# Optimization experiments

Measured on AMD Instinct MI355X. Metric: run time of the kernel, lower is better.

Reference implementation:

```python
import jax, jax.numpy as jnp
import numpy as np

D_MODEL = 2048
NUM_Q_HEADS = 32
NUM_KV_HEADS = 8
HEAD_DIM = D_MODEL // NUM_Q_HEADS  # 64
NUM_GROUPS = NUM_Q_HEADS // NUM_KV_HEADS  # 4


def setup_inputs() -> dict:
    key = jax.random.key(0)
    ks = jax.random.split(key, 9)
    s = 1.0 / np.sqrt(D_MODEL)
    x = jax.random.normal(ks[0], (2, 2048, D_MODEL), dtype=jnp.float32)
    Wq = jax.random.uniform(ks[1], (D_MODEL, NUM_Q_HEADS * HEAD_DIM), jnp.float32, -s, s)
    bq = jax.random.uniform(ks[2], (NUM_Q_HEADS * HEAD_DIM,), jnp.float32, -s, s)
    Wk = jax.random.uniform(ks[3], (D_MODEL, NUM_KV_HEADS * HEAD_DIM), jnp.float32, -s, s)
    bk = jax.random.uniform(ks[4], (NUM_KV_HEADS * HEAD_DIM,), jnp.float32, -s, s)
    Wv = jax.random.uniform(ks[5], (D_MODEL, NUM_KV_HEADS * HEAD_DIM), jnp.float32, -s, s)
    bv = jax.random.uniform(ks[6], (NUM_KV_HEADS * HEAD_DIM,), jnp.float32, -s, s)
    Wo = jax.random.uniform(ks[7], (D_MODEL, D_MODEL), jnp.float32, -s, s)
    bo = jax.random.uniform(ks[8], (D_MODEL,), jnp.float32, -s, s)
    return {"x": x, "Wq": Wq, "bq": bq, "Wk": Wk, "bk": bk,
            "Wv": Wv, "bv": bv, "Wo": Wo, "bo": bo}


def reference(x, Wq, bq, Wk, bk, Wv, bv, Wo, bo):
    B, T, C = x.shape
    Hkv, G, Dh = NUM_KV_HEADS, NUM_GROUPS, HEAD_DIM
    # projections
    q = (x @ Wq + bq).reshape(B, T, Hkv, G, Dh)   # group G query heads per kv head
    k = (x @ Wk + bk).reshape(B, T, Hkv, Dh)
    v = (x @ Wv + bv).reshape(B, T, Hkv, Dh)
    scale = 1.0 / np.sqrt(Dh).astype(np.float32)
    # scores: [B, Hkv, G, T, T] (kv head broadcast over its G query heads)
    scores = jnp.einsum('btkgd,bskd->bkgts', q, k) * scale
    attn = jax.nn.softmax(scores, axis=-1)
    out = jnp.einsum('bkgts,bskd->btkgd', attn, v).reshape(B, T, C)
    return out @ Wo + bo
```

## Files before the change

kernel.cpp:

```cpp
#include <hip/hip_runtime.h>
#include <cstdint>
#include <cstddef>
#include <math.h>

typedef uint16_t bf16;
typedef __attribute__((ext_vector_type(8))) __bf16 bf16x8;
typedef __attribute__((ext_vector_type(2))) float f32x2;
typedef __attribute__((ext_vector_type(4))) float f32x4;
typedef __attribute__((ext_vector_type(16))) float f32x16;

#define MFMA16(a,b,c) __builtin_amdgcn_mfma_f32_16x16x32_bf16((a),(b),(c),0,0,0)
#define MFMA32(a,b,c) __builtin_amdgcn_mfma_f32_32x32x16_bf16((a),(b),(c),0,0,0)

__device__ __forceinline__ uint16_t f2bf(float f){
  uint32_t u = __float_as_uint(f);
  return (uint16_t)((u + 0x7fffu + ((u >> 16) & 1u)) >> 16);
}
__device__ __forceinline__ uint32_t pk2(float lo, float hi){
  return (uint32_t)f2bf(lo) | ((uint32_t)f2bf(hi) << 16);
}

__device__ __forceinline__ void gload_lds16(const void* g, void* l){
  __builtin_amdgcn_global_load_lds((const __attribute__((address_space(1))) void*)g,
                                   (__attribute__((address_space(3))) void*)l, 16, 0, 0);
}

__global__ void k_convert(const float* __restrict__ in, bf16* __restrict__ out, int n){
  int i = (blockIdx.x * 256 + threadIdx.x) * 4;
  if (i >= n) return;
  float4 v = *reinterpret_cast<const float4*>(in + i);
  uint32_t lo = pk2(v.x, v.y);
  uint32_t hi = pk2(v.z, v.w);
  uint2 pkv = make_uint2(lo, hi);
  *reinterpret_cast<uint2*>(out + i) = pkv;
}

__global__ void k_transposeW(const float* __restrict__ in, bf16* __restrict__ out, int R, int C){
  __shared__ float tile[64][65];
  int c0 = blockIdx.x * 64, r0 = blockIdx.y * 64;
  int t = threadIdx.x;
  int fx = t & 15, fy = t >> 4;
  #pragma unroll
  for (int i = 0; i < 4; i++){
    int r = fy + i*16;
    float4 v = *reinterpret_cast<const float4*>(in + (size_t)(r0 + r)*C + c0 + fx*4);
    tile[r][fx*4+0] = v.x; tile[r][fx*4+1] = v.y;
    tile[r][fx*4+2] = v.z; tile[r][fx*4+3] = v.w;
  }
  __syncthreads();
  int gx = t & 7, gy = t >> 3;
  #pragma unroll
  for (int i = 0; i < 2; i++){
    int c = gy + i*32;
    int rr = gx*8;
    union { bf16 h[8]; uint4 u; } pk_;
    #pragma unroll
    for (int j = 0; j < 8; j++) pk_.h[j] = f2bf(tile[rr+j][c]);
    *reinterpret_cast<uint4*>(out + (size_t)(c0 + c)*R + r0 + rr) = pk_.u;
  }
}

__device__ __forceinline__ void gemm128_core(
    const bf16* __restrict__ Abase, const bf16* __restrict__ Btbase,
    int lda, int ldb, int K, bf16* As, bf16* Bs, f32x4 acc[4][4])
{
  const int tid = threadIdx.x;
  const int wid = tid >> 6, lane = tid & 63;
  const int wr = wid >> 1, wc = wid & 1;
  const int lr = lane & 15, lg = lane >> 4;
  const f32x4 vzero = {0.f, 0.f, 0.f, 0.f};

  #pragma unroll
  for (int m = 0; m < 4; m++)
    #pragma unroll
    for (int n = 0; n < 4; n++)
      acc[m][n] = vzero;

  int srcA[4], srcB[4], dOff[4];
  #pragma unroll
  for (int i = 0; i < 4; i++){
    int d = i*4096 + wid*1024 + lane*16;
    int row = d >> 7, sp = (d >> 4) & 7;
    int sl = sp ^ (row & 7);
    srcA[i] = row * lda + sl * 8;
    srcB[i] = row * ldb + sl * 8;
    dOff[i] = i*4096 + wid*1024;
  }

  for (int k0 = 0; k0 < K; k0 += 64){
    #pragma unroll
    for (int i = 0; i < 4; i++)
      gload_lds16(Abase + k0 + srcA[i], (char*)As + dOff[i]);
    #pragma unroll
    for (int i = 0; i < 4; i++)
      gload_lds16(Btbase + k0 + srcB[i], (char*)Bs + dOff[i]);
    __syncthreads();
    #pragma unroll
    for (int ks = 0; ks < 2; ks++){
      bf16x8 af[4], bfr[4];
      #pragma unroll
      for (int m = 0; m < 4; m++){
        int row = wr*64 + m*16 + lr;
        int sp = (ks*4 + lg) ^ (row & 7);
        af[m] = *reinterpret_cast<const bf16x8*>(As + row*64 + sp*8);
      }
      #pragma unroll
      for (int n = 0; n < 4; n++){
        int row = wc*64 + n*16 + lr;
        int sp = (ks*4 + lg) ^ (row & 7);
        bfr[n] = *reinterpret_cast<const bf16x8*>(Bs + row*64 + sp*8);
      }
      #pragma unroll
      for (int m = 0; m < 4; m++)
        #pragma unroll
        for (int n = 0; n < 4; n++)
          acc[m][n] = MFMA16(af[m], bfr[n], acc[m][n]);
    }
    __syncthreads();
  }
}

__global__ __launch_bounds__(256, 2) void k_qkv(
    const bf16* __restrict__ xb,
    const bf16* __restrict__ WqT, const bf16* __restrict__ WkT, const bf16* __restrict__ WvT,
    const float* __restrict__ bq, const float* __restrict__ bk, const float* __restrict__ bv,
    bf16* __restrict__ qo, bf16* __restrict__ ko, bf16* __restrict__ vtp)
{
  __shared__ __align__(16) bf16 As[128*64];
  __shared__ __align__(16) bf16 Bs[128*64];
  int by = blockIdx.y;
  const bf16* Bt; const float* bias; int mode; int y = 0; float scale = 1.f;
  if (by < 16){      Bt = WqT + (size_t)by*128*2048;      bias = bq + by*128; mode = 0; y = by;   scale = 0.18033688011112042f; }
  else if (by < 20){ y = by-16; Bt = WkT + (size_t)y*128*2048; bias = bk + y*128; mode = 1; }
  else {             y = by-20; Bt = WvT + (size_t)y*128*2048; bias = bv + y*128; mode = 2; }
  int m0 = blockIdx.x * 128;
  f32x4 acc[4][4];
  gemm128_core(xb + (size_t)m0*2048, Bt, 2048, 2048, 2048, As, Bs, acc);
  const int tid = threadIdx.x, wid = tid >> 6, lane = tid & 63;
  const int wr = wid >> 1, wc = wid & 1, lr = lane & 15, lg = lane >> 4;
  if (mode == 2){
    #pragma unroll
    for (int n = 0; n < 4; n++){
      int cl = wc*64 + n*16 + lr;
      float bb = bias[cl];
      #pragma unroll
      for (int m = 0; m < 4; m++){
        int row0 = m0 + wr*64 + m*16 + lg*4;
        int bi = row0 >> 11, tl = row0 & 2047;
        union { bf16 h[4]; uint2 u; } pk_;
        #pragma unroll
        for (int r = 0; r < 4; r++) pk_.h[r] = f2bf(acc[m][n][r] + bb);
        *reinterpret_cast<uint2*>(vtp + ((size_t)bi*512 + y*128 + cl)*2048 + tl) = pk_.u;
      }
    }
  } else {
    bf16* outp = (mode == 0) ? (qo + y*128) : (ko + y*128);
    int ldc = (mode == 0) ? 2048 : 512;
    #pragma unroll
    for (int n = 0; n < 4; n++){
      int col = wc*64 + n*16 + lr;
      float bb = bias[col];
      #pragma unroll
      for (int m = 0; m < 4; m++)
        #pragma unroll
        for (int r = 0; r < 4; r++){
          int row = m0 + wr*64 + m*16 + lg*4 + r;
          outp[(size_t)row*ldc + col] = f2bf((acc[m][n][r] + bb) * scale);
        }
    }
  }
}

__global__ __launch_bounds__(256, 2) void k_oproj(
    const bf16* __restrict__ ab, const bf16* __restrict__ WoT,
    const float* __restrict__ bo, float* __restrict__ outp)
{
  __shared__ __align__(16) bf16 As[128*64];
  __shared__ __align__(16) bf16 Bs[128*64];
  int m0 = blockIdx.x * 128, n0 = blockIdx.y * 128;
  f32x4 acc[4][4];
  gemm128_core(ab + (size_t)m0*2048, WoT + (size_t)n0*2048, 2048, 2048, 2048, As, Bs, acc);
  const int tid = threadIdx.x, wid = tid >> 6, lane = tid & 63;
  const int wr = wid >> 1, wc = wid & 1, lr = lane & 15, lg = lane >> 4;
  #pragma unroll
  for (int n = 0; n < 4; n++){
    int col = n0 + wc*64 + n*16 + lr;
    float bb = bo[col];
    #pragma unroll
    for (int m = 0; m < 4; m++)
      #pragma unroll
      for (int r = 0; r < 4; r++){
        int row = m0 + wr*64 + m*16 + lg*4 + r;
        outp[(size_t)row*2048 + col] = acc[m][n][r] + bb;
      }
  }
}

__global__ __launch_bounds__(512, 2) void k_flash(
    const bf16* __restrict__ q, const bf16* __restrict__ kmat,
    const bf16* __restrict__ vt, bf16* __restrict__ ao)
{
  __shared__ __align__(16) char lds[98304];
  const int tid = threadIdx.x;
  const int wid = tid >> 6, lane = tid & 63;
  const int l31 = lane & 31, hi = lane >> 5;
  const int bh = blockIdx.y;
  const int b = bh >> 5, hq = bh & 31, kvh = hq >> 2;
  const int qt = blockIdx.x;
  const int qrow0 = b*2048 + qt*512 + wid*64;

  bf16x8 qf[2][4];
  #pragma unroll
  for (int g = 0; g < 2; g++){
    const bf16* qrow = q + (size_t)(qrow0 + g*32 + l31)*2048 + hq*64 + hi*8;
    #pragma unroll
    for (int t = 0; t < 4; t++)
      qf[g][t] = *reinterpret_cast<const bf16x8*>(qrow + t*16);
  }

  f32x16 oacc[2][2];
  #pragma unroll
  for (int g = 0; g < 2; g++)
    #pragma unroll
    for (int n = 0; n < 2; n++)
      #pragma unroll
      for (int r = 0; r < 16; r++) oacc[g][n][r] = 0.f;
  float rsg[2][2];
  rsg[0][0]=0.f; rsg[0][1]=0.f; rsg[1][0]=0.f; rsg[1][1]=0.f;
  const f32x16 zv = {0.f,0.f,0.f,0.f,0.f,0.f,0.f,0.f,0.f,0.f,0.f,0.f,0.f,0.f,0.f,0.f};

  const int r7 = l31 & 7;
  int A[4];
  #pragma unroll
  for (int j = 0; j < 4; j++)
    A[j] = l31*128 + (((2*j + hi) ^ r7) << 4);

  const bf16* kbase = kmat + (size_t)b*2048*512 + kvh*64;
  const bf16* vbase = vt + ((size_t)b*512 + kvh*64)*2048;

  int kSrc[2], vSrc[2];
  const int dOf = wid*1024;
  #pragma unroll
  for (int i = 0; i < 2; i++){
    int kdb = i*8192 + tid*16;
    int krow = kdb >> 7, ksp = (kdb >> 4) & 7, ksl = ksp ^ (krow & 7);
    kSrc[i] = krow*512 + ksl*8;
    int o = tid*16;
    int vrow = o >> 7, vsp = (o >> 4) & 7, vsl = vsp ^ (vrow & 7);
    vSrc[i] = vrow*2048 + i*64 + vsl*8;
  }

  #define STAGE(bo, st_) do { \
    const bf16* kb_ = kbase + (size_t)(st_)*128*512; \
    const bf16* vb_ = vbase + (st_)*128; \
    gload_lds16(kb_ + kSrc[0], lds + (bo) + dOf); \
    gload_lds16(kb_ + kSrc[1], lds + (bo) + 8192 + dOf); \
    gload_lds16(vb_ + vSrc[0], lds + 49152 + (bo) + dOf); \
    gload_lds16(vb_ + vSrc[1], lds + 49152 + (bo) + 8192 + dOf); \
  } while(0)

  #define LDK(j, imm) (*reinterpret_cast<const bf16x8*>(lds + kOff + A[j] + (imm)))
  #define LDV(j, imm) (*reinterpret_cast<const bf16x8*>(lds + 49152 + kOff + A[j] + (imm)))

  STAGE(0, 0);
  STAGE(16384, 1);

  int kOff = 0;
  int sOff = 32768;
  for (int st = 0; st < 16; st++){
    if (st == 15) asm volatile("s_waitcnt vmcnt(0)" ::: "memory");
    else          asm volatile("s_waitcnt vmcnt(4)" ::: "memory");
    __builtin_amdgcn_sched_barrier(0);
    __builtin_amdgcn_s_barrier();
    __builtin_amdgcn_sched_barrier(0);
    if (st < 14){
      STAGE(sOff, st+2);
      sOff = (sOff == 32768) ? 0 : sOff + 16384;
    }

    #pragma unroll
    for (int c = 0; c < 2; c++){
      f32x16 sc[2][2];
      __builtin_amdgcn_s_setprio(1);
      #pragma unroll
      for (int t = 0; t < 4; t++){
        bf16x8 af0 = LDK(t, c*8192);
        bf16x8 af1 = LDK(t, c*8192 + 4096);
        if (t == 0){
          sc[0][0] = MFMA32(af0, qf[0][0], zv);
          sc[1][0] = MFMA32(af0, qf[1][0], zv);
          sc[0][1] = MFMA32(af1, qf[0][0], zv);
          sc[1][1] = MFMA32(af1, qf[1][0], zv);
        } else {
          sc[0][0] = MFMA32(af0, qf[0][t], sc[0][0]);
          sc[1][0] = MFMA32(af0, qf[1][t], sc[1][0]);
          sc[0][1] = MFMA32(af1, qf[0][t], sc[0][1]);
          sc[1][1] = MFMA32(af1, qf[1][t], sc[1][1]);
        }
      }
      __builtin_amdgcn_s_setprio(0);

      uint32_t pw[2][2][8];
      #pragma unroll
      for (int g = 0; g < 2; g++){
        #pragma unroll
        for (int n = 0; n < 2; n++)
          #pragma unroll
          for (int j = 0; j < 8; j++){
            float plo = __builtin_amdgcn_exp2f(sc[g][n][2*j]);
            float phi = __builtin_amdgcn_exp2f(sc[g][n][2*j+1]);
            rsg[g][j & 1] += plo + phi;
            asm("v_cvt_pk_bf16_f32 %0, %1, %2" : "=v"(pw[g][n][j]) : "v"(plo), "v"(phi));
          }
        #pragma unroll
        for (int n = 0; n < 2; n++)
          #pragma unroll
          for (int h = 0; h < 2; h++){
            asm volatile("v_permlane32_swap_b32 %0, %1" : "+v"(pw[g][n][h*4+0]), "+v"(pw[g][n][h*4+2]));
            asm volatile("v_permlane32_swap_b32 %0, %1" : "+v"(pw[g][n][h*4+1]), "+v"(pw[g][n][h*4+3]));
          }
      }

      __builtin_amdgcn_s_setprio(1);
      #pragma unroll
      for (int kk = 0; kk < 4; kk++){
        int n = kk >> 1, h = kk & 1;
        union { uint32_t w[4]; bf16x8 v; } pa0, pa1;
        #pragma unroll
        for (int w_ = 0; w_ < 4; w_++){ pa0.w[w_] = pw[0][n][h*4+w_]; pa1.w[w_] = pw[1][n][h*4+w_]; }
        #pragma unroll
        for (int nd = 0; nd < 2; nd++){
          bf16x8 vf = LDV(kk, c*8192 + nd*4096);
          oacc[0][nd] = MFMA32(pa0.v, vf, oacc[0][nd]);
          oacc[1][nd] = MFMA32(pa1.v, vf, oacc[1][nd]);
        }
      }
      __builtin_amdgcn_s_setprio(0);
    }
    kOff = (kOff == 32768) ? 0 : kOff + 16384;
  }
  #undef STAGE
  #undef LDK
  #undef LDV

  #pragma unroll
  for (int g = 0; g < 2; g++){
    float rs = rsg[g][0] + rsg[g][1];
    float l = rs + __shfl_xor(rs, 32);
    float linv = 1.f / l;
    float lv[16];
    #pragma unroll
    for (int r = 0; r < 16; r++){
      int qi = (r & 3) + 8*(r >> 2) + 4*hi;
      lv[r] = __shfl(linv, qi);
    }
    #pragma unroll
    for (int nd = 0; nd < 2; nd++)
      #pragma unroll
      for (int r = 0; r < 16; r++){
        int qi = (r & 3) + 8*(r >> 2) + 4*hi;
        int row = qrow0 + g*32 + qi;
        ao[(size_t)row*2048 + hq*64 + nd*32 + l31] = f2bf(oacc[g][nd][r] * lv[r]);
      }
  }
}

extern "C" void kernel_launch(void* const* d_in, const int* in_sizes, int n_in,
                              void* d_out, int out_size, void* d_ws, size_t ws_size,
                              hipStream_t stream)
{
  const float* x  = (const float*)d_in[0];
  const float* Wq = (const float*)d_in[1];
  const float* bq = (const float*)d_in[2];
  const float* Wk = (const float*)d_in[3];
  const float* bk = (const float*)d_in[4];
  const float* Wv = (const float*)d_in[5];
  const float* bv = (const float*)d_in[6];
  const float* Wo = (const float*)d_in[7];
  const float* bo = (const float*)d_in[8];
  float* out = (float*)d_out;

  char* ws = (char*)d_ws;
  size_t off = 0;
  auto alloc = [&](size_t bytes){ char* p = ws + off; off += (bytes + 255) & ~(size_t)255; return p; };
  bf16* xb  = (bf16*)alloc(2*2048*2048*2);
  bf16* WqT = (bf16*)alloc(2048*2048*2);
  bf16* WkT = (bf16*)alloc(512*2048*2);
  bf16* WvT = (bf16*)alloc(512*2048*2);
  bf16* WoT = (bf16*)alloc(2048*2048*2);
  bf16* qb  = (bf16*)alloc(4096*2048*2);
  bf16* kb  = (bf16*)alloc((size_t)4096*512*2);
  bf16* vtb = (bf16*)alloc((size_t)4096*512*2);
  bf16* aob = xb;

  k_convert<<<8192, 256, 0, stream>>>(x, xb, 2*2048*2048);
  k_transposeW<<<dim3(32,32), 256, 0, stream>>>(Wq, WqT, 2048, 2048);
  k_transposeW<<<dim3(8,32),  256, 0, stream>>>(Wk, WkT, 2048, 512);
  k_transposeW<<<dim3(8,32),  256, 0, stream>>>(Wv, WvT, 2048, 512);
  k_transposeW<<<dim3(32,32), 256, 0, stream>>>(Wo, WoT, 2048, 2048);
  k_qkv<<<dim3(32,24), 256, 0, stream>>>(xb, WqT, WkT, WvT, bq, bk, bv, qb, kb, vtb);
  k_flash<<<dim3(4,64), 512, 0, stream>>>(qb, kb, vtb, aob);
  k_oproj<<<dim3(32,16), 256, 0, stream>>>(aob, WoT, bo, out);
}
```

Baseline: 193.8 us.

## Double-buffer GEMM core with 8-wave 128x256 tiles and interleaved prefetch

```diff
diff --git a/kernel.cpp b/kernel.cpp
--- a/kernel.cpp
+++ b/kernel.cpp
@@ -60,84 +60,127 @@
   }
 }
 
-__device__ __forceinline__ void gemm128_core(
+__device__ __forceinline__ void gemm8_core(
     const bf16* __restrict__ Abase, const bf16* __restrict__ Btbase,
-    int lda, int ldb, int K, bf16* As, bf16* Bs, f32x4 acc[4][4])
+    char* lds, f32x4 acc[4][4])
 {
   const int tid = threadIdx.x;
   const int wid = tid >> 6, lane = tid & 63;
-  const int wr = wid >> 1, wc = wid & 1;
+  const int wr = wid >> 2, wc = wid & 3;
   const int lr = lane & 15, lg = lane >> 4;
   const f32x4 vzero = {0.f, 0.f, 0.f, 0.f};
-
   #pragma unroll
   for (int m = 0; m < 4; m++)
     #pragma unroll
     for (int n = 0; n < 4; n++)
       acc[m][n] = vzero;
 
-  int srcA[4], srcB[4], dOff[4];
+  int srcA[2], srcB[4];
+  #pragma unroll
+  for (int i = 0; i < 2; i++){
+    int db = i*8192 + tid*16;
+    int row = db >> 7, sp = (db >> 4) & 7, sl = sp ^ (row & 7);
+    srcA[i] = row*2048 + sl*8;
+  }
   #pragma unroll
   for (int i = 0; i < 4; i++){
-    int d = i*4096 + wid*1024 + lane*16;
-    int row = d >> 7, sp = (d >> 4) & 7;
-    int sl = sp ^ (row & 7);
-    srcA[i] = row * lda + sl * 8;
-    srcB[i] = row * ldb + sl * 8;
-    dOff[i] = i*4096 + wid*1024;
-  }
-
-  for (int k0 = 0; k0 < K; k0 += 64){
-    #pragma unroll
-    for (int i = 0; i < 4; i++)
-      gload_lds16(Abase + k0 + srcA[i], (char*)As + dOff[i]);
-    #pragma unroll
-    for (int i = 0; i < 4; i++)
-      gload_lds16(Btbase + k0 + srcB[i], (char*)Bs + dOff[i]);
-    __syncthreads();
-    #pragma unroll
-    for (int ks = 0; ks < 2; ks++){
-      bf16x8 af[4], bfr[4];
-      #pragma unroll
-      for (int m = 0; m < 4; m++){
-        int row = wr*64 + m*16 + lr;
-        int sp = (ks*4 + lg) ^ (row & 7);
-        af[m] = *reinterpret_cast<const bf16x8*>(As + row*64 + sp*8);
-      }
-      #pragma unroll
-      for (int n = 0; n < 4; n++){
-        int row = wc*64 + n*16 + lr;
-        int sp = (ks*4 + lg) ^ (row & 7);
-        bfr[n] = *reinterpret_cast<const bf16x8*>(Bs + row*64 + sp*8);
-      }
-      #pragma unroll
-      for (int m = 0; m < 4; m++)
-        #pragma unroll
-        for (int n = 0; n < 4; n++)
-          acc[m][n] = MFMA16(af[m], bfr[n], acc[m][n]);
-    }
-    __syncthreads();
-  }
-}
-
-__global__ __launch_bounds__(256, 2) void k_qkv(
+    int db = i*8192 + tid*16;
+    int row = db >> 7, sp = (db >> 4) & 7, sl = sp ^ (row & 7);
+    srcB[i] = row*2048 + sl*8;
+  }
+  const int dOf = wid*1024;
+
+  int aAddr[4][2], bAddr[4][2];
+  #pragma unroll
+  for (int m = 0; m < 4; m++){
+    int row = wr*64 + m*16 + lr;
+    #pragma unroll
+    for (int ks = 0; ks < 2; ks++)
+      aAddr[m][ks] = row*128 + (((ks*4 + lg) ^ (row & 7)) << 4);
+  }
+  #pragma unroll
+  for (int n = 0; n < 4; n++){
+    int row = wc*64 + n*16 + lr;
+    #pragma unroll
+    for (int ks = 0; ks < 2; ks++)
+      bAddr[n][ks] = 32768 + row*128 + (((ks*4 + lg) ^ (row & 7)) << 4);
+  }
+
+  #pragma unroll
+  for (int i = 0; i < 2; i++) gload_lds16(Abase + srcA[i], lds + i*8192 + dOf);
+  #pragma unroll
+  for (int i = 0; i < 4; i++) gload_lds16(Btbase + srcB[i], lds + 32768 + i*8192 + dOf);
+  asm volatile("s_waitcnt vmcnt(0)" ::: "memory");
+  __builtin_amdgcn_s_barrier();
+
+  for (int t = 0; t < 32; t++){
+    const int ct = t & 1;
+    const int nx = ct ^ 1;
+    const int aOff = ct*16384, bOff = ct*32768;
+    const bf16* An = Abase + (t+1)*64;
+    const bf16* Bn = Btbase + (t+1)*64;
+    #pragma unroll
+    for (int q = 0; q < 4; q++){
+      const int qm = q >> 1, qn = q & 1;
+      bf16x8 af[2][2], bfv[2][2];
+      #pragma unroll
+      for (int mm = 0; mm < 2; mm++)
+        #pragma unroll
+        for (int ks = 0; ks < 2; ks++)
+          af[mm][ks] = *reinterpret_cast<const bf16x8*>(lds + aOff + aAddr[qm*2+mm][ks]);
+      #pragma unroll
+      for (int nn = 0; nn < 2; nn++)
+        #pragma unroll
+        for (int ks = 0; ks < 2; ks++)
+          bfv[nn][ks] = *reinterpret_cast<const bf16x8*>(lds + bOff + bAddr[qn*2+nn][ks]);
+      if (t < 31){
+        if (q == 0){
+          gload_lds16(An + srcA[0], lds + nx*16384 + dOf);
+          gload_lds16(An + srcA[1], lds + nx*16384 + 8192 + dOf);
+        } else if (q == 1){
+          gload_lds16(Bn + srcB[0], lds + 32768 + nx*32768 + dOf);
+          gload_lds16(Bn + srcB[1], lds + 32768 + nx*32768 + 8192 + dOf);
+        } else if (q == 2){
+          gload_lds16(Bn + srcB[2], lds + 32768 + nx*32768 + 16384 + dOf);
+          gload_lds16(Bn + srcB[3], lds + 32768 + nx*32768 + 24576 + dOf);
+        }
+      }
+      __builtin_amdgcn_s_barrier();
+      asm volatile("s_waitcnt lgkmcnt(0)" ::: "memory");
+      __builtin_amdgcn_sched_barrier(0);
+      __builtin_amdgcn_s_setprio(1);
+      #pragma unroll
+      for (int mm = 0; mm < 2; mm++)
+        #pragma unroll
+        for (int nn = 0; nn < 2; nn++)
+          #pragma unroll
+          for (int ks = 0; ks < 2; ks++)
+            acc[qm*2+mm][qn*2+nn] = MFMA16(af[mm][ks], bfv[nn][ks], acc[qm*2+mm][qn*2+nn]);
+      __builtin_amdgcn_s_setprio(0);
+      if (q == 3 && t < 31)
+        asm volatile("s_waitcnt vmcnt(0)" ::: "memory");
+      __builtin_amdgcn_s_barrier();
+    }
+  }
+}
+
+__global__ __launch_bounds__(512, 1) void k_qkv(
     const bf16* __restrict__ xb,
     const bf16* __restrict__ WqT, const bf16* __restrict__ WkT, const bf16* __restrict__ WvT,
     const float* __restrict__ bq, const float* __restrict__ bk, const float* __restrict__ bv,
     bf16* __restrict__ qo, bf16* __restrict__ ko, bf16* __restrict__ vtp)
 {
-  __shared__ __align__(16) bf16 As[128*64];
-  __shared__ __align__(16) bf16 Bs[128*64];
+  __shared__ __align__(16) char lds[98304];
   int by = blockIdx.y;
-  const bf16* Bt; const float* bias; int mode; int y = 0; float scale = 1.f;
-  if (by < 16){      Bt = WqT + (size_t)by*128*2048;      bias = bq + by*128; mode = 0; y = by;   scale = 0.18033688011112042f; }
-  else if (by < 20){ y = by-16; Bt = WkT + (size_t)y*128*2048; bias = bk + y*128; mode = 1; }
-  else {             y = by-20; Bt = WvT + (size_t)y*128*2048; bias = bv + y*128; mode = 2; }
+  const bf16* Bt; const float* bias; int mode; int y; float scale = 1.f;
+  if (by < 8){       y = by;    Bt = WqT + (size_t)y*256*2048; bias = bq + y*256; mode = 0; scale = 0.18033688011112042f; }
+  else if (by < 10){ y = by-8;  Bt = WkT + (size_t)y*256*2048; bias = bk + y*256; mode = 1; }
+  else {             y = by-10; Bt = WvT + (size_t)y*256*2048; bias = bv + y*256; mode = 2; }
   int m0 = blockIdx.x * 128;
   f32x4 acc[4][4];
-  gemm128_core(xb + (size_t)m0*2048, Bt, 2048, 2048, 2048, As, Bs, acc);
+  gemm8_core(xb + (size_t)m0*2048, Bt, lds, acc);
   const int tid = threadIdx.x, wid = tid >> 6, lane = tid & 63;
-  const int wr = wid >> 1, wc = wid & 1, lr = lane & 15, lg = lane >> 4;
+  const int wr = wid >> 2, wc = wid & 3, lr = lane & 15, lg = lane >> 4;
   if (mode == 2){
     #pragma unroll
     for (int n = 0; n < 4; n++){
@@ -150,11 +193,11 @@
         union { bf16 h[4]; uint2 u; } pk_;
         #pragma unroll
         for (int r = 0; r < 4; r++) pk_.h[r] = f2bf(acc[m][n][r] + bb);
-        *reinterpret_cast<uint2*>(vtp + ((size_t)bi*512 + y*128 + cl)*2048 + tl) = pk_.u;
+        *reinterpret_cast<uint2*>(vtp + ((size_t)bi*512 + y*256 + cl)*2048 + tl) = pk_.u;
       }
     }
   } else {
-    bf16* outp = (mode == 0) ? (qo + y*128) : (ko + y*128);
+    bf16* outp = (mode == 0) ? (qo + y*256) : (ko + y*256);
     int ldc = (mode == 0) ? 2048 : 512;
     #pragma unroll
     for (int n = 0; n < 4; n++){
@@ -171,17 +214,16 @@
   }
 }
 
-__global__ __launch_bounds__(256, 2) void k_oproj(
+__global__ __launch_bounds__(512, 1) void k_oproj(
     const bf16* __restrict__ ab, const bf16* __restrict__ WoT,
     const float* __restrict__ bo, float* __restrict__ outp)
 {
-  __shared__ __align__(16) bf16 As[128*64];
-  __shared__ __align__(16) bf16 Bs[128*64];
-  int m0 = blockIdx.x * 128, n0 = blockIdx.y * 128;
+  __shared__ __align__(16) char lds[98304];
+  int m0 = blockIdx.x * 128, n0 = blockIdx.y * 256;
   f32x4 acc[4][4];
-  gemm128_core(ab + (size_t)m0*2048, WoT + (size_t)n0*2048, 2048, 2048, 2048, As, Bs, acc);
+  gemm8_core(ab + (size_t)m0*2048, WoT + (size_t)n0*2048, lds, acc);
   const int tid = threadIdx.x, wid = tid >> 6, lane = tid & 63;
-  const int wr = wid >> 1, wc = wid & 1, lr = lane & 15, lg = lane >> 4;
+  const int wr = wid >> 2, wc = wid & 3, lr = lane & 15, lg = lane >> 4;
   #pragma unroll
   for (int n = 0; n < 4; n++){
     int col = n0 + wc*64 + n*16 + lr;
@@ -398,7 +440,7 @@
   k_transposeW<<<dim3(8,32),  256, 0, stream>>>(Wk, WkT, 2048, 512);
   k_transposeW<<<dim3(8,32),  256, 0, stream>>>(Wv, WvT, 2048, 512);
   k_transposeW<<<dim3(32,32), 256, 0, stream>>>(Wo, WoT, 2048, 2048);
-  k_qkv<<<dim3(32,24), 256, 0, stream>>>(xb, WqT, WkT, WvT, bq, bk, bv, qb, kb, vtb);
+  k_qkv<<<dim3(32,12), 512, 0, stream>>>(xb, WqT, WkT, WvT, bq, bk, bv, qb, kb, vtb);
   k_flash<<<dim3(4,64), 512, 0, stream>>>(qb, kb, vtb, aob);
-  k_oproj<<<dim3(32,16), 256, 0, stream>>>(aob, WoT, bo, out);
-}
+  k_oproj<<<dim3(32,8), 512, 0, stream>>>(aob, WoT, bo, out);
+}
```

Result: slower. 218.5 us (+12.7%).

## Use 256x256 tile GEMM with staged LDS prefetch for QKV projection

Applied to the files above, without the earlier changes.

```diff
diff --git a/kernel.cpp b/kernel.cpp
--- a/kernel.cpp
+++ b/kernel.cpp
@@ -120,52 +120,187 @@
   }
 }
 
-__global__ __launch_bounds__(256, 2) void k_qkv(
+__device__ __forceinline__ void gemm256_core(
+    const bf16* __restrict__ Abase, const bf16* __restrict__ Btbase,
+    char* lds, f32x4 acc[8][4])
+{
+  const int tid = threadIdx.x;
+  const int wid = tid >> 6, lane = tid & 63;
+  const int wm = wid >> 2, wn = wid & 3;
+  const int lr = lane & 15, lg = lane >> 4;
+  const f32x4 vzero = {0.f, 0.f, 0.f, 0.f};
+  #pragma unroll
+  for (int m = 0; m < 8; m++)
+    #pragma unroll
+    for (int n = 0; n < 4; n++)
+      acc[m][n] = vzero;
+
+  int srcH[2];
+  #pragma unroll
+  for (int i = 0; i < 2; i++){
+    int db = i*8192 + tid*16;
+    int row = db >> 7, sp = (db >> 4) & 7, sl = sp ^ (row & 7);
+    srcH[i] = row*2048 + sl*8;
+  }
+  const int dOf = wid*1024;
+
+  int ksl[2];
+  #pragma unroll
+  for (int ks = 0; ks < 2; ks++) ksl[ks] = (((ks*4 + lg) ^ (lr & 7)) << 4);
+  const int aB = wm*16384 + lr*128;
+  const int bB = 32768 + (wn >> 1)*16384 + (wn & 1)*8192 + lr*128;
+
+  const bf16* Ab1 = Abase + 128*2048;
+  const bf16* Bb1 = Btbase + 128*2048;
+
+  #define STG_HALF(dstOff, gsrc) do { \
+    gload_lds16((gsrc) + srcH[0], lds + (dstOff) + dOf); \
+    gload_lds16((gsrc) + srcH[1], lds + (dstOff) + 8192 + dOf); \
+  } while(0)
+
+  STG_HALF(0,     Abase);
+  STG_HALF(16384, Ab1);
+  STG_HALF(32768, Btbase);
+  STG_HALF(49152, Bb1);
+  STG_HALF(65536, Abase + 64);
+  asm volatile("s_waitcnt vmcnt(2)" ::: "memory");
+  __builtin_amdgcn_s_barrier();
+
+  bf16x8 afr[4][2], bfr[4][2];
+  for (int t = 0; t < 32; t++){
+    const int bo = (t & 1) * 65536;
+    const int nb = bo ^ 65536;
+
+    #pragma unroll
+    for (int am = 0; am < 4; am++)
+      #pragma unroll
+      for (int ks = 0; ks < 2; ks++)
+        afr[am][ks] = *reinterpret_cast<const bf16x8*>(lds + bo + aB + am*2048 + ksl[ks]);
+    #pragma unroll
+    for (int bn = 0; bn < 2; bn++)
+      #pragma unroll
+      for (int ks = 0; ks < 2; ks++)
+        bfr[bn][ks] = *reinterpret_cast<const bf16x8*>(lds + bo + bB + bn*2048 + ksl[ks]);
+    if (t < 31) STG_HALF(nb + 16384, Ab1 + (t+1)*64);
+    __builtin_amdgcn_s_barrier();
+    asm volatile("s_waitcnt lgkmcnt(0)" ::: "memory");
+    __builtin_amdgcn_sched_barrier(0);
+    __builtin_amdgcn_s_setprio(1);
+    #pragma unroll
+    for (int am = 0; am < 4; am++)
+      #pragma unroll
+      for (int bn = 0; bn < 2; bn++)
+        #pragma unroll
+        for (int ks = 0; ks < 2; ks++)
+          acc[am][bn] = MFMA16(afr[am][ks], bfr[bn][ks], acc[am][bn]);
+    __builtin_amdgcn_s_setprio(0);
+    __builtin_amdgcn_s_barrier();
+
+    #pragma unroll
+    for (int bn = 2; bn < 4; bn++)
+      #pragma unroll
+      for (int ks = 0; ks < 2; ks++)
+        bfr[bn][ks] = *reinterpret_cast<const bf16x8*>(lds + bo + bB + bn*2048 + ksl[ks]);
+    if (t < 31) STG_HALF(nb + 32768, Btbase + (t+1)*64);
+    __builtin_amdgcn_s_barrier();
+    asm volatile("s_waitcnt lgkmcnt(0)" ::: "memory");
+    __builtin_amdgcn_sched_barrier(0);
+    __builtin_amdgcn_s_setprio(1);
+    #pragma unroll
+    for (int am = 0; am < 4; am++)
+      #pragma unroll
+      for (int bn = 2; bn < 4; bn++)
+        #pragma unroll
+        for (int ks = 0; ks < 2; ks++)
+          acc[am][bn] = MFMA16(afr[am][ks], bfr[bn][ks], acc[am][bn]);
+    __builtin_amdgcn_s_setprio(0);
+    __builtin_amdgcn_s_barrier();
+
+    #pragma unroll
+    for (int am = 0; am < 4; am++)
+      #pragma unroll
+      for (int ks = 0; ks < 2; ks++)
+        afr[am][ks] = *reinterpret_cast<const bf16x8*>(lds + bo + aB + (am+4)*2048 + ksl[ks]);
+    if (t < 31) STG_HALF(nb + 49152, Bb1 + (t+1)*64);
+    __builtin_amdgcn_s_barrier();
+    asm volatile("s_waitcnt lgkmcnt(0)" ::: "memory");
+    __builtin_amdgcn_sched_barrier(0);
+    __builtin_amdgcn_s_setprio(1);
+    #pragma unroll
+    for (int am = 0; am < 4; am++)
+      #pragma unroll
+      for (int bn = 0; bn < 2; bn++)
+        #pragma unroll
+        for (int ks = 0; ks < 2; ks++)
+          acc[am+4][bn] = MFMA16(afr[am][ks], bfr[bn][ks], acc[am+4][bn]);
+    __builtin_amdgcn_s_setprio(0);
+    __builtin_amdgcn_s_barrier();
+
+    if (t < 30) STG_HALF(bo, Abase + (t+2)*64);
+    __builtin_amdgcn_s_barrier();
+    __builtin_amdgcn_s_setprio(1);
+    #pragma unroll
+    for (int am = 0; am < 4; am++)
+      #pragma unroll
+      for (int bn = 2; bn < 4; bn++)
+        #pragma unroll
+        for (int ks = 0; ks < 2; ks++)
+          acc[am+4][bn] = MFMA16(afr[am][ks], bfr[bn][ks], acc[am+4][bn]);
+    __builtin_amdgcn_s_setprio(0);
+    if (t < 30)      asm volatile("s_waitcnt vmcnt(2)" ::: "memory");
+    else if (t == 30) asm volatile("s_waitcnt vmcnt(0)" ::: "memory");
+    __builtin_amdgcn_sched_barrier(0);
+    __builtin_amdgcn_s_barrier();
+  }
+  #undef STG_HALF
+}
+
+__global__ __launch_bounds__(512, 1) void k_qkv(
     const bf16* __restrict__ xb,
     const bf16* __restrict__ WqT, const bf16* __restrict__ WkT, const bf16* __restrict__ WvT,
     const float* __restrict__ bq, const float* __restrict__ bk, const float* __restrict__ bv,
     bf16* __restrict__ qo, bf16* __restrict__ ko, bf16* __restrict__ vtp)
 {
-  __shared__ __align__(16) bf16 As[128*64];
-  __shared__ __align__(16) bf16 Bs[128*64];
+  __shared__ __align__(16) char lds[131072];
   int by = blockIdx.y;
-  const bf16* Bt; const float* bias; int mode; int y = 0; float scale = 1.f;
-  if (by < 16){      Bt = WqT + (size_t)by*128*2048;      bias = bq + by*128; mode = 0; y = by;   scale = 0.18033688011112042f; }
-  else if (by < 20){ y = by-16; Bt = WkT + (size_t)y*128*2048; bias = bk + y*128; mode = 1; }
-  else {             y = by-20; Bt = WvT + (size_t)y*128*2048; bias = bv + y*128; mode = 2; }
-  int m0 = blockIdx.x * 128;
-  f32x4 acc[4][4];
-  gemm128_core(xb + (size_t)m0*2048, Bt, 2048, 2048, 2048, As, Bs, acc);
+  const bf16* Bt; const float* bias; int mode; int y; float scale = 1.f;
+  if (by < 8){       y = by;    Bt = WqT + (size_t)y*256*2048; bias = bq + y*256; mode = 0; scale = 0.18033688011112042f; }
+  else if (by < 10){ y = by-8;  Bt = WkT + (size_t)y*256*2048; bias = bk + y*256; mode = 1; }
+  else {             y = by-10; Bt = WvT + (size_t)y*256*2048; bias = bv + y*256; mode = 2; }
+  int m0 = blockIdx.x * 256;
+  f32x4 acc[8][4];
+  gemm256_core(xb + (size_t)m0*2048, Bt, lds, acc);
   const int tid = threadIdx.x, wid = tid >> 6, lane = tid & 63;
-  const int wr = wid >> 1, wc = wid & 1, lr = lane & 15, lg = lane >> 4;
+  const int wm = wid >> 2, wn = wid & 3, lr = lane & 15, lg = lane >> 4;
   if (mode == 2){
     #pragma unroll
-    for (int n = 0; n < 4; n++){
-      int cl = wc*64 + n*16 + lr;
-      float bb = bias[cl];
-      #pragma unroll
-      for (int m = 0; m < 4; m++){
-        int row0 = m0 + wr*64 + m*16 + lg*4;
+    for (int bn = 0; bn < 4; bn++){
+      int c = wn*64 + bn*16 + lr;
+      float bb = bias[c];
+      int CL = y*256 + c;
+      #pragma unroll
+      for (int am = 0; am < 8; am++){
+        int row0 = m0 + wm*128 + am*16 + lg*4;
         int bi = row0 >> 11, tl = row0 & 2047;
         union { bf16 h[4]; uint2 u; } pk_;
         #pragma unroll
-        for (int r = 0; r < 4; r++) pk_.h[r] = f2bf(acc[m][n][r] + bb);
-        *reinterpret_cast<uint2*>(vtp + ((size_t)bi*512 + y*128 + cl)*2048 + tl) = pk_.u;
+        for (int r = 0; r < 4; r++) pk_.h[r] = f2bf(acc[am][bn][r] + bb);
+        *reinterpret_cast<uint2*>(vtp + ((size_t)bi*512 + CL)*2048 + tl) = pk_.u;
       }
     }
   } else {
-    bf16* outp = (mode == 0) ? (qo + y*128) : (ko + y*128);
+    bf16* outp = (mode == 0) ? (qo + y*256) : (ko + y*256);
     int ldc = (mode == 0) ? 2048 : 512;
     #pragma unroll
-    for (int n = 0; n < 4; n++){
-      int col = wc*64 + n*16 + lr;
-      float bb = bias[col];
-      #pragma unroll
-      for (int m = 0; m < 4; m++)
+    for (int bn = 0; bn < 4; bn++){
+      int c = wn*64 + bn*16 + lr;
+      float bb = bias[c];
+      #pragma unroll
+      for (int am = 0; am < 8; am++)
         #pragma unroll
         for (int r = 0; r < 4; r++){
-          int row = m0 + wr*64 + m*16 + lg*4 + r;
-          outp[(size_t)row*ldc + col] = f2bf((acc[m][n][r] + bb) * scale);
+          int row = m0 + wm*128 + am*16 + lg*4 + r;
+          outp[(size_t)row*ldc + c] = f2bf((acc[am][bn][r] + bb) * scale);
         }
     }
   }
@@ -398,7 +533,7 @@
   k_transposeW<<<dim3(8,32),  256, 0, stream>>>(Wk, WkT, 2048, 512);
   k_transposeW<<<dim3(8,32),  256, 0, stream>>>(Wv, WvT, 2048, 512);
   k_transposeW<<<dim3(32,32), 256, 0, stream>>>(Wo, WoT, 2048, 2048);
-  k_qkv<<<dim3(32,24), 256, 0, stream>>>(xb, WqT, WkT, WvT, bq, bk, bv, qb, kb, vtb);
+  k_qkv<<<dim3(16,12), 512, 0, stream>>>(xb, WqT, WkT, WvT, bq, bk, bv, qb, kb, vtb);
   k_flash<<<dim3(4,64), 512, 0, stream>>>(qb, kb, vtb, aob);
   k_oproj<<<dim3(32,16), 256, 0, stream>>>(aob, WoT, bo, out);
 }
```

New measurement: 194.3 us. No clear change (+0.2%).
